# Kernel optimization log

Hardware: AMD Instinct MI355X
Metric: run time of the kernel (lower is better)

Reference implementation:

```python
import jax, jax.numpy as jnp
import numpy as np

N = 8192
K = 64
EPS = 1e-7
BN_EPS = 1e-5


def _norm(x):
    return jnp.sqrt(jnp.sum(x * x, axis=-1, keepdims=True))


def _bn(x, gamma, beta):
    # BatchNorm2d in training mode (batch statistics, biased variance)
    mu = jnp.mean(x, axis=(0, 2, 3), keepdims=True)
    var = jnp.mean((x - mu) ** 2, axis=(0, 2, 3), keepdims=True)
    return gamma.reshape(1, -1, 1, 1) * (x - mu) / jnp.sqrt(var + BN_EPS) + beta.reshape(1, -1, 1, 1)


def _conv1x1(x, w, b):
    # 1x1 conv == per-pixel linear: x [B,C,H,W], w [O,C]
    return jnp.einsum('bchw,oc->bohw', x, w) + b.reshape(1, -1, 1, 1)


def setup_inputs() -> dict:
    key = jax.random.key(0)
    ks = jax.random.split(key, 24)
    d = {}
    d['points'] = jax.random.normal(ks[0], (1, N, 3), jnp.float32)
    # graph_conv weights (torch code re-draws these every forward; here fixed params)
    lim0 = float(np.sqrt(6.0 / (4 + 64)))
    d['gw0'] = jax.random.uniform(ks[1], (4, 64), jnp.float32, -lim0, lim0)
    lim = float(np.sqrt(6.0 / (64 + 64)))
    for i in range(1, 5):
        d[f'gw{i}'] = jax.random.uniform(ks[1 + i], (64, 64), jnp.float32, -lim, lim)
    # mlp_1: 4->64->128, mlp_2: 192->256->1024 (1x1 convs + BN)
    d['c1w'] = jax.random.normal(ks[6], (64, 4), jnp.float32) * 0.1
    d['c1b'] = jnp.zeros((64,), jnp.float32)
    d['bn1g'] = jnp.ones((64,), jnp.float32)
    d['bn1b'] = jnp.zeros((64,), jnp.float32)
    d['c2w'] = jax.random.normal(ks[7], (128, 64), jnp.float32) * 0.1
    d['c2b'] = jnp.zeros((128,), jnp.float32)
    d['bn2g'] = jnp.ones((128,), jnp.float32)
    d['bn2b'] = jnp.zeros((128,), jnp.float32)
    d['c3w'] = jax.random.normal(ks[8], (256, 192), jnp.float32) * 0.05
    d['c3b'] = jnp.zeros((256,), jnp.float32)
    d['bn3g'] = jnp.ones((256,), jnp.float32)
    d['bn3b'] = jnp.zeros((256,), jnp.float32)
    d['c4w'] = jax.random.normal(ks[9], (1024, 256), jnp.float32) * 0.05
    d['c4b'] = jnp.zeros((1024,), jnp.float32)
    d['bn4g'] = jnp.ones((1024,), jnp.float32)
    d['bn4b'] = jnp.zeros((1024,), jnp.float32)
    return d


def _knn_search(points, k):
    # pairwise squared distances via ||a||^2 - 2ab + ||b||^2
    r = jnp.sum(points * points, axis=-1, keepdims=True)          # [1,N,1]
    dis = r - 2.0 * jnp.einsum('bnd,bmd->bnm', points, points) + jnp.swapaxes(r, 1, 2)
    _, idx = jax.lax.top_k(-dis, k)                                # [1,N,K]
    knn_pts = jax.vmap(lambda p, i: p[i])(points, idx)             # [1,N,K,3]
    return knn_pts


def _proj_knn(knn_pts):
    b, n, k, _ = knn_pts.shape
    pc = knn_pts - knn_pts[:, :, :1, :]                            # center on first neighbor (self)
    vn = jnp.sqrt(jnp.sum(pc * pc, axis=-1))                       # [1,N,K]
    id1 = jnp.argmax(vn, axis=-1)                                  # farthest neighbor
    a1 = jnp.take_along_axis(pc, jnp.broadcast_to(id1[:, :, None, None], (b, n, 1, 3)), axis=2)[:, :, 0, :]
    a1 = a1 / (_norm(a1) + EPS)
    a2 = jnp.mean(pc, axis=2)
    a2 = a2 / (_norm(a2) + EPS)
    a3 = a1 + 1.5 * a2
    a3 = a3 / (_norm(a3) + EPS)
    den = _norm(pc) + EPS                                          # [1,N,K,1]
    f1 = jnp.sum(pc * a1[:, :, None, :], axis=-1, keepdims=True) / den
    f2 = jnp.sum(pc * a2[:, :, None, :], axis=-1, keepdims=True) / den
    f3 = jnp.sum(pc * a3[:, :, None, :], axis=-1, keepdims=True) / den
    return jnp.concatenate([f1, f2, f3, vn[..., None]], axis=-1)   # [1,N,K,4]


def _proj_points(points):
    b, n, _ = points.shape
    vn = jnp.sqrt(jnp.sum(points * points, axis=-1))               # [1,N]
    i1 = jnp.argmax(vn, axis=-1)
    i2 = jnp.argmin(vn, axis=-1)
    a1 = jnp.take_along_axis(points, jnp.broadcast_to(i1[:, None, None], (b, 1, 3)), axis=1)[:, 0, :]
    a1 = a1 / (_norm(a1) + EPS)
    a2 = jnp.take_along_axis(points, jnp.broadcast_to(i2[:, None, None], (b, 1, 3)), axis=1)[:, 0, :]
    a2 = a2 / (_norm(a2) + EPS)
    a3 = a1 + 1.5 * a2
    a3 = a3 / (_norm(a3) + EPS)
    den = _norm(points) + EPS                                      # [1,N,1]
    f1 = jnp.sum(points * a1[:, None, :], axis=-1, keepdims=True) / den
    f2 = jnp.sum(points * a2[:, None, :], axis=-1, keepdims=True) / den
    f3 = jnp.sum(points * a3[:, None, :], axis=-1, keepdims=True) / den
    return jnp.concatenate([f1, f2, f3, vn[..., None]], axis=-1)   # [1,N,4]


def reference(points, gw0, gw1, gw2, gw3, gw4,
              c1w, c1b, bn1g, bn1b, c2w, c2b, bn2g, bn2b,
              c3w, c3b, bn3g, bn3b, c4w, c4b, bn4g, bn4b):
    n = points.shape[1]
    # upper branch: KNN -> rotation-invariant local feats -> 5-layer MLP -> max over K
    knn_pts = _knn_search(points, K)
    feat_up = _proj_knn(knn_pts)                                   # [1,N,K,4]
    x = feat_up.reshape(-1, 4)
    for w in (gw0, gw1, gw2, gw3, gw4):
        x = jax.nn.relu(x @ w)
    x = x.reshape(1, n, K, 64)
    emb_up = jnp.max(x, axis=2, keepdims=True)                     # [1,N,1,64]
    emb_up = emb_up.reshape(1, 64, n, 1)                           # raw view (reshape), as in torch
    # lower branch: global rotation-invariant feats -> mlp_1
    feat_down = _proj_points(points)                               # [1,N,4]
    emb_down = feat_down.reshape(1, 4, n, 1)                       # raw view (reshape), as in torch
    h = jax.nn.relu(_bn(_conv1x1(emb_down, c1w, c1b), bn1g, bn1b))
    h = jax.nn.relu(_bn(_conv1x1(h, c2w, c2b), bn2g, bn2b))        # [1,128,N,1]
    emb = jnp.concatenate([emb_up, h], axis=1)                     # [1,192,N,1]
    out = jax.nn.relu(_bn(_conv1x1(emb, c3w, c3b), bn3g, bn3b))
    out = jax.nn.relu(_bn(_conv1x1(out, c4w, c4b), bn4g, bn4b))    # [1,1024,N,1]
    return out
```

## Files before the change

### kernel.cpp

```cpp
#include <hip/hip_runtime.h>
#include <hip/hip_bf16.h>

#define NPTS 8192
#define KNN 64
#define EPSF 1e-7f

#define OFF_P4      0
#define OFF_STATS   32768
#define OFF_PART    36012
#define OFF_FEATDN  36864
#define OFF_WT1     69632
#define OFF_GWT     69888
#define OFF_BW2     79104
#define OFF_BW3     83200
#define OFF_BW4     107776
#define OFF_XB1     238848
#define OFF_XB3     500992
#define OFF_XB4     1287424
#define OFF_Y1      2336000
#define OFF_Y2      2860288
#define OFF_Y3      3908864
#define OFF_FEATUP  6006016

typedef __bf16 bf16x8 __attribute__((ext_vector_type(8)));
typedef float  f32x4  __attribute__((ext_vector_type(4)));

__device__ __forceinline__ unsigned f2u(float f) {
    unsigned u = __float_as_uint(f);
    return ((int)u >= 0) ? (u | 0x80000000u) : ~u;
}
__device__ __forceinline__ float key_to_f(unsigned long long k) {
    unsigned v = (unsigned)(k >> 32);
    unsigned ob = (v & 0x80000000u) ? (v ^ 0x80000000u) : ~v;
    return __uint_as_float(ob);
}
__device__ __forceinline__ unsigned short f2bf(float x) {
    union { __bf16 h; unsigned short s; } u;
    u.h = (__bf16)x;
    return u.s;
}
__device__ __forceinline__ unsigned packbf2(float lo, float hi) {
    return (unsigned)f2bf(lo) | ((unsigned)f2bf(hi) << 16);
}
__device__ __forceinline__ unsigned long long u64min(unsigned long long a, unsigned long long b){ return a < b ? a : b; }
__device__ __forceinline__ unsigned long long u64max(unsigned long long a, unsigned long long b){ return a < b ? b : a; }

__device__ __forceinline__ unsigned long long sort_merge(
    unsigned long long key, unsigned long long cur, int lane)
{
    #pragma unroll
    for (int k = 2; k <= 64; k <<= 1) {
        #pragma unroll
        for (int j = k >> 1; j > 0; j >>= 1) {
            unsigned long long o = __shfl_xor(key, j);
            bool up = ((lane & k) == 0);
            bool lower = ((lane & j) == 0);
            key = (lower == up) ? u64min(key, o) : u64max(key, o);
        }
    }
    unsigned long long rev = __shfl(key, 63 - lane);
    unsigned long long m = u64min(cur, rev);
    #pragma unroll
    for (int j = 32; j > 0; j >>= 1) {
        unsigned long long o = __shfl_xor(m, j);
        m = ((lane & j) == 0) ? u64min(m, o) : u64max(m, o);
    }
    return m;
}

__global__ __launch_bounds__(256) void prepwt_kernel(
    const float* __restrict__ points,
    const float* __restrict__ c1w, const float* __restrict__ c2w,
    const float* __restrict__ c3w, const float* __restrict__ c4w,
    const float* __restrict__ gw0, const float* __restrict__ gw1,
    const float* __restrict__ gw2, const float* __restrict__ gw3,
    const float* __restrict__ gw4,
    float* __restrict__ ws)
{
    const int t = blockIdx.x * 256 + threadIdx.x;
    const int T = 256 * 256;
    for (int m = t; m < 2944; m += T) ws[OFF_STATS + m] = 0.f;
    for (int m = t; m < 64*4; m += T) { int o = m >> 2, c = m & 3; ws[OFF_WT1 + c*64 + o] = c1w[m]; }

    unsigned short* bw2 = (unsigned short*)(ws + OFF_BW2);
    for (int m = t; m < 128*64; m += T)   bw2[m] = f2bf(c2w[m]);
    unsigned short* bw3 = (unsigned short*)(ws + OFF_BW3);
    for (int m = t; m < 256*192; m += T)  bw3[m] = f2bf(c3w[m]);
    unsigned short* bw4 = (unsigned short*)(ws + OFF_BW4);
    for (int m = t; m < 1024*256; m += T) bw4[m] = f2bf(c4w[m]);

    unsigned short* gwt = (unsigned short*)(ws + OFF_GWT);
    for (int m = t; m < 2048; m += T) {
        int o = m >> 5, i = m & 31;
        gwt[m] = (i < 4) ? f2bf(gw0[i*64 + o]) : (unsigned short)0;
    }
    const float* gsrc[4] = {gw1, gw2, gw3, gw4};
    for (int l = 0; l < 4; ++l) {
        const float* g = gsrc[l];
        unsigned short* dst = gwt + 2048 + l*4096;
        for (int m = t; m < 4096; m += T) { int o = m >> 6, i = m & 63; dst[m] = f2bf(g[i*64 + o]); }
    }

    if (blockIdx.x < 32) {
        const int n = blockIdx.x * 256 + threadIdx.x;
        float x = points[3*n+0], y = points[3*n+1], z = points[3*n+2];
        float rr = x*x + y*y + z*z;
        ((float4*)(ws + OFF_P4))[n] = make_float4(x, y, z, rr);
        float vn = sqrtf(rr);
        unsigned b = __float_as_uint(vn);
        unsigned long long mxk = ((unsigned long long)b << 32) | (unsigned long long)(0xFFFFFFFFu - (unsigned)n);
        unsigned long long mnk = ((unsigned long long)b << 32) | (unsigned long long)(unsigned)n;
        for (int j = 32; j > 0; j >>= 1) {
            mxk = u64max(mxk, __shfl_xor(mxk, j));
            mnk = u64min(mnk, __shfl_xor(mnk, j));
        }
        __shared__ unsigned long long smx[4], smn[4];
        int wid = threadIdx.x >> 6;
        if ((threadIdx.x & 63) == 0) { smx[wid] = mxk; smn[wid] = mnk; }
        __syncthreads();
        if (threadIdx.x == 0) {
            unsigned long long MX = 0ull, MN = ~0ull;
            for (int i = 0; i < 4; ++i) { MX = u64max(MX, smx[i]); MN = u64min(MN, smn[i]); }
            unsigned long long* parts = (unsigned long long*)(ws + OFF_PART);
            parts[2*blockIdx.x + 0] = MX;
            parts[2*blockIdx.x + 1] = MN;
        }
    }
}

__global__ __launch_bounds__(256) void prep_c_kernel(float* __restrict__ ws)
{
    __shared__ float av[9];
    const int tid = threadIdx.x;
    if (tid < 64) {
        const unsigned long long* parts = (const unsigned long long*)(ws + OFF_PART);
        unsigned long long mxk = (tid < 32) ? parts[2*tid + 0] : 0ull;
        unsigned long long mnk = (tid < 32) ? parts[2*tid + 1] : ~0ull;
        for (int j = 32; j > 0; j >>= 1) {
            mxk = u64max(mxk, __shfl_xor(mxk, j));
            mnk = u64min(mnk, __shfl_xor(mnk, j));
        }
        if (tid == 0) {
            int i1 = (int)(0xFFFFFFFFu - (unsigned)(mxk & 0xFFFFFFFFu));
            int i2 = (int)(unsigned)(mnk & 0xFFFFFFFFu);
            float4 p1 = ((const float4*)(ws + OFF_P4))[i1];
            float4 p2 = ((const float4*)(ws + OFF_P4))[i2];
            float n1 = sqrtf(p1.x*p1.x + p1.y*p1.y + p1.z*p1.z) + EPSF;
            float a1x = p1.x/n1, a1y = p1.y/n1, a1z = p1.z/n1;
            float n2 = sqrtf(p2.x*p2.x + p2.y*p2.y + p2.z*p2.z) + EPSF;
            float a2x = p2.x/n2, a2y = p2.y/n2, a2z = p2.z/n2;
            float a3x = a1x + 1.5f*a2x, a3y = a1y + 1.5f*a2y, a3z = a1z + 1.5f*a2z;
            float n3 = sqrtf(a3x*a3x + a3y*a3y + a3z*a3z) + EPSF;
            a3x /= n3; a3y /= n3; a3z /= n3;
            av[0]=a1x; av[1]=a1y; av[2]=a1z;
            av[3]=a2x; av[4]=a2y; av[5]=a2z;
            av[6]=a3x; av[7]=a3y; av[8]=a3z;
        }
    }
    __syncthreads();
    const int n = blockIdx.x * 256 + tid;
    float4 v = ((const float4*)(ws + OFF_P4))[n];
    float vn = sqrtf(v.w);
    float den = vn + EPSF;
    float f1 = (v.x*av[0] + v.y*av[1] + v.z*av[2]) / den;
    float f2 = (v.x*av[3] + v.y*av[4] + v.z*av[5]) / den;
    float f3 = (v.x*av[6] + v.y*av[7] + v.z*av[8]) / den;
    float4* f4 = (float4*)(ws + OFF_FEATDN + 4*n);
    *f4 = make_float4(f1, f2, f3, vn);
}

__global__ __launch_bounds__(512) void knn_feat_kernel(
    const float4* __restrict__ p4, float4* __restrict__ feat_up)
{
    __shared__ __align__(16) float4 scand[2048];
    __shared__ unsigned long long queue[8][128];
    const int lane = threadIdx.x & 63;
    const int wid  = threadIdx.x >> 6;
    const int q = blockIdx.x * 8 + wid;

    const float4 qa = p4[q];
    unsigned long long cur = ~0ull;
    float ke = __builtin_inff();
    int qc = 0;
    unsigned long long* Q = queue[wid];

    for (int base = 0; base < NPTS; base += 2048) {
        __syncthreads();
        for (int t = threadIdx.x; t < 2048; t += 512) scand[t] = p4[base + t];
        __syncthreads();
        #pragma unroll 2
        for (int sub = 0; sub < 2048; sub += 128) {
            float4 cd0 = scand[sub + lane];
            float4 cd1 = scand[sub + 64 + lane];
            float dot0 = fmaf(qa.x, cd0.x, fmaf(qa.y, cd0.y, qa.z * cd0.z));
            float dot1 = fmaf(qa.x, cd1.x, fmaf(qa.y, cd1.y, qa.z * cd1.z));
            float e0 = fmaf(-2.f, dot0, cd0.w);
            float e1 = fmaf(-2.f, dot1, cd1.w);
            bool p0 = e0 < ke;
            bool p1 = e1 < ke;
            unsigned long long m0 = __ballot(p0);
            unsigned long long m1 = __ballot(p1);
            if (m0) {
                int prefix = __builtin_amdgcn_mbcnt_hi((unsigned)(m0 >> 32),
                              __builtin_amdgcn_mbcnt_lo((unsigned)m0, 0));
                if (p0) Q[qc + prefix] = ((unsigned long long)f2u(e0) << 32)
                                       | (unsigned long long)(unsigned)(base + sub + lane);
                qc += __popcll(m0);
                if (qc >= 64) {
                    qc -= 64;
                    cur = sort_merge(Q[qc + lane], cur, lane);
                    ke = key_to_f(__shfl(cur, 63));
                }
            }
            if (m1) {
                int prefix = __builtin_amdgcn_mbcnt_hi((unsigned)(m1 >> 32),
                              __builtin_amdgcn_mbcnt_lo((unsigned)m1, 0));
                if (p1) Q[qc + prefix] = ((unsigned long long)f2u(e1) << 32)
                                       | (unsigned long long)(unsigned)(base + sub + 64 + lane);
                qc += __popcll(m1);
                if (qc >= 64) {
                    qc -= 64;
                    cur = sort_merge(Q[qc + lane], cur, lane);
                    ke = key_to_f(__shfl(cur, 63));
                }
            }
        }
    }
    cur = sort_merge((lane < qc) ? Q[lane] : ~0ull, cur, lane);

    int nidx = (int)(unsigned)(cur & 0xFFFFFFFFu);
    float4 np = p4[nidx];
    float ox = __shfl(np.x, 0), oy = __shfl(np.y, 0), oz = __shfl(np.z, 0);
    float pcx = np.x - ox, pcy = np.y - oy, pcz = np.z - oz;
    float vn = sqrtf(pcx*pcx + pcy*pcy + pcz*pcz);

    unsigned long long ak = ((unsigned long long)__float_as_uint(vn) << 32)
                          | (unsigned long long)(unsigned)(63 - lane);
    for (int s = 32; s > 0; s >>= 1) ak = u64max(ak, __shfl_xor(ak, s));
    int id1 = 63 - (int)(unsigned)(ak & 0xFFFFFFFFu);

    float a1x = __shfl(pcx, id1), a1y = __shfl(pcy, id1), a1z = __shfl(pcz, id1);
    float n1 = sqrtf(a1x*a1x + a1y*a1y + a1z*a1z) + EPSF;
    a1x /= n1; a1y /= n1; a1z /= n1;

    float sx = pcx, sy = pcy, sz = pcz;
    for (int s = 32; s > 0; s >>= 1) {
        sx += __shfl_xor(sx, s); sy += __shfl_xor(sy, s); sz += __shfl_xor(sz, s);
    }
    float a2x = sx * (1.f/64.f), a2y = sy * (1.f/64.f), a2z = sz * (1.f/64.f);
    float n2 = sqrtf(a2x*a2x + a2y*a2y + a2z*a2z) + EPSF;
    a2x /= n2; a2y /= n2; a2z /= n2;

    float a3x = a1x + 1.5f*a2x, a3y = a1y + 1.5f*a2y, a3z = a1z + 1.5f*a2z;
    float n3 = sqrtf(a3x*a3x + a3y*a3y + a3z*a3z) + EPSF;
    a3x /= n3; a3y /= n3; a3z /= n3;

    float den = vn + EPSF;
    float f1 = (pcx*a1x + pcy*a1y + pcz*a1z) / den;
    float f2 = (pcx*a2x + pcy*a2y + pcz*a2z) / den;
    float f3 = (pcx*a3x + pcy*a3y + pcz*a3z) / den;
    feat_up[q*64 + lane] = make_float4(f1, f2, f3, vn);
}

#define BROW 72
__global__ __launch_bounds__(256) void mlp_kernel(
    const float4* __restrict__ feat_up,
    const unsigned short* __restrict__ gwt,
    unsigned short* __restrict__ xb3)
{
    __shared__ __align__(16) unsigned short Blds[4][64 * BROW];
    const int lane = threadIdx.x & 63;
    const int wid  = threadIdx.x >> 6;
    const int q = blockIdx.x * 4 + wid;
    const int c = lane & 15, g = lane >> 4;
    unsigned short* B = Blds[wid];

    {
        float4 f = feat_up[q*64 + lane];
        uint2 p0;
        p0.x = packbf2(f.x, f.y);
        p0.y = packbf2(f.z, f.w);
        *(uint2*)&B[lane*BROW] = p0;
        *(uint2*)&B[lane*BROW + 4] = make_uint2(0, 0);
        uint4 z4 = make_uint4(0, 0, 0, 0);
        *(uint4*)&B[lane*BROW + 8]  = z4;
        *(uint4*)&B[lane*BROW + 16] = z4;
        *(uint4*)&B[lane*BROW + 24] = z4;
    }

    const unsigned short* Wl[5] = {gwt, gwt + 2048, gwt + 6144, gwt + 10240, gwt + 14336};
    f32x4 acc[4][4];

    for (int layer = 0; layer < 5; ++layer) {
        const int wstride = (layer == 0) ? 32 : 64;
        const int nks = (layer == 0) ? 1 : 2;
        #pragma unroll
        for (int mb = 0; mb < 4; ++mb)
            #pragma unroll
            for (int nb = 0; nb < 4; ++nb)
                acc[mb][nb] = (f32x4){0.f, 0.f, 0.f, 0.f};

        for (int ks = 0; ks < nks; ++ks) {
            bf16x8 af[4], bf[4];
            #pragma unroll
            for (int mb = 0; mb < 4; ++mb)
                af[mb] = *(const bf16x8*)(Wl[layer] + (mb*16 + c)*wstride + ks*32 + g*8);
            #pragma unroll
            for (int nb = 0; nb < 4; ++nb)
                bf[nb] = *(const bf16x8*)&B[(nb*16 + c)*BROW + ks*32 + g*8];
            #pragma unroll
            for (int mb = 0; mb < 4; ++mb)
                #pragma unroll
                for (int nb = 0; nb < 4; ++nb)
                    acc[mb][nb] = __builtin_amdgcn_mfma_f32_16x16x32_bf16(af[mb], bf[nb], acc[mb][nb], 0, 0, 0);
        }

        if (layer < 4) {
            #pragma unroll
            for (int mb = 0; mb < 4; ++mb) {
                #pragma unroll
                for (int nb = 0; nb < 4; ++nb) {
                    f32x4 a = acc[mb][nb];
                    uint2 pw;
                    pw.x = packbf2(fmaxf(a[0], 0.f), fmaxf(a[1], 0.f));
                    pw.y = packbf2(fmaxf(a[2], 0.f), fmaxf(a[3], 0.f));
                    *(uint2*)&B[(nb*16 + c)*BROW + mb*16 + g*4] = pw;
                }
            }
        }
    }

    const int cc = q >> 7;
    const int pbase = (q & 127) << 6;
    #pragma unroll
    for (int mb = 0; mb < 4; ++mb) {
        float v[4];
        #pragma unroll
        for (int r = 0; r < 4; ++r)
            v[r] = fmaxf(fmaxf(fmaxf(acc[mb][0][r], acc[mb][1][r]),
                               fmaxf(acc[mb][2][r], acc[mb][3][r])), 0.f);
        #pragma unroll
        for (int mask = 1; mask <= 8; mask <<= 1)
            #pragma unroll
            for (int r = 0; r < 4; ++r)
                v[r] = fmaxf(v[r], __shfl_xor(v[r], mask));
        if (c == 0) {
            #pragma unroll
            for (int r = 0; r < 4; ++r) {
                const int f = mb*16 + g*4 + r;
                xb3[(size_t)(pbase + f) * 192 + cc] = f2bf(v[r]);
            }
        }
    }
}

__global__ __launch_bounds__(256) void conv1_kernel(
    const float* __restrict__ x, const float* __restrict__ wt,
    const float* __restrict__ bias, float* __restrict__ y,
    float* __restrict__ stout)
{
    const int tid = threadIdx.x;
    const int p  = blockIdx.x * 256 + tid;
    const int o0 = blockIdx.y * 32;
    float acc[32];
    #pragma unroll
    for (int u = 0; u < 32; ++u) acc[u] = bias[o0 + u];
    #pragma unroll
    for (int c = 0; c < 4; ++c) {
        float xv = x[c * NPTS + p];
        const float* wr = wt + c * 64 + o0;
        #pragma unroll
        for (int u = 0; u < 32; ++u) acc[u] = fmaf(xv, wr[u], acc[u]);
    }
    #pragma unroll
    for (int u = 0; u < 32; ++u) y[(o0 + u) * NPTS + p] = acc[u];

    __shared__ float ps[4][32], pss[4][32];
    const int wid = tid >> 6, lane = tid & 63;
    #pragma unroll
    for (int u = 0; u < 32; ++u) {
        float s = acc[u], ss = acc[u] * acc[u];
        for (int j = 32; j > 0; j >>= 1) { s += __shfl_xor(s, j); ss += __shfl_xor(ss, j); }
        if (lane == 0) { ps[wid][u] = s; pss[wid][u] = ss; }
    }
    __syncthreads();
    if (tid < 32) {
        float S  = ps[0][tid] + ps[1][tid] + ps[2][tid] + ps[3][tid];
        float SS = pss[0][tid] + pss[1][tid] + pss[2][tid] + pss[3][tid];
        atomicAdd(&stout[o0 + tid], S);
        atomicAdd(&stout[64 + o0 + tid], SS);
    }
}

__global__ __launch_bounds__(256) void bnpack_kernel(
    const float* __restrict__ y, const float* __restrict__ st,
    const float* __restrict__ gam, const float* __restrict__ bet,
    int C, int stride, int coff, unsigned short* __restrict__ xb)
{
    __shared__ float sc[256], sh[256];
    __shared__ __align__(16) unsigned short tile[64][264];
    const int tid = threadIdx.x;
    for (int cc = tid; cc < C; cc += 256) {
        float mu  = st[cc] * (1.f / 8192.f);
        float var = st[C + cc] * (1.f / 8192.f) - mu * mu;
        float s = gam[cc] / sqrtf(var + 1e-5f);
        sc[cc] = s; sh[cc] = bet[cc] - mu * s;
    }
    __syncthreads();
    const int pl = tid & 63, g = tid >> 6;
    const int p = blockIdx.x * 64 + pl;
    for (int c0 = g * 8; c0 < C; c0 += 32) {
        unsigned pk[4];
        #pragma unroll
        for (int h = 0; h < 4; ++h) {
            float v0 = fmaxf(fmaf(y[(c0 + 2*h    ) * NPTS + p], sc[c0 + 2*h    ], sh[c0 + 2*h    ]), 0.f);
            float v1 = fmaxf(fmaf(y[(c0 + 2*h + 1) * NPTS + p], sc[c0 + 2*h + 1], sh[c0 + 2*h + 1]), 0.f);
            pk[h] = packbf2(v0, v1);
        }
        *(uint4*)&tile[pl][c0] = make_uint4(pk[0], pk[1], pk[2], pk[3]);
    }
    __syncthreads();
    const int cpr = C >> 3;
    const int nch = 64 * cpr;
    for (int idx = tid; idx < nch; idx += 256) {
        int r = idx / cpr, cc = (idx - r * cpr) * 8;
        *(uint4*)&xb[(size_t)(blockIdx.x * 64 + r) * stride + coff + cc] = *(uint4*)&tile[r][cc];
    }
}

__global__ __launch_bounds__(256) void conv_mfma_kernel(
    const unsigned short* __restrict__ A, const unsigned short* __restrict__ Bx,
    const float* __restrict__ bias, int K, int M,
    float* __restrict__ y, float* __restrict__ stout)
{
    const int lane = threadIdx.x & 63;
    const int w = threadIdx.x >> 6;
    const int n0 = blockIdx.x * 256 + w * 64;
    const int m0 = blockIdx.y * 64;
    const int c = lane & 15, g = lane >> 4;

    f32x4 acc[4][4];
    #pragma unroll
    for (int mt = 0; mt < 4; ++mt)
        #pragma unroll
        for (int nt = 0; nt < 4; ++nt)
            acc[mt][nt] = (f32x4){0.f, 0.f, 0.f, 0.f};

    for (int k0 = 0; k0 < K; k0 += 32) {
        bf16x8 af[4], bf[4];
        #pragma unroll
        for (int mt = 0; mt < 4; ++mt)
            af[mt] = *(const bf16x8*)(A + (size_t)(m0 + mt*16 + c) * K + k0 + g*8);
        #pragma unroll
        for (int nt = 0; nt < 4; ++nt)
            bf[nt] = *(const bf16x8*)(Bx + (size_t)(n0 + nt*16 + c) * K + k0 + g*8);
        #pragma unroll
        for (int mt = 0; mt < 4; ++mt)
            #pragma unroll
            for (int nt = 0; nt < 4; ++nt)
                acc[mt][nt] = __builtin_amdgcn_mfma_f32_16x16x32_bf16(af[mt], bf[nt], acc[mt][nt], 0, 0, 0);
    }

    #pragma unroll
    for (int mt = 0; mt < 4; ++mt) {
        float s[4], ss[4];
        #pragma unroll
        for (int r = 0; r < 4; ++r) {
            const int o = m0 + mt*16 + g*4 + r;
            const float bv = bias[o];
            float sum = 0.f, sq = 0.f;
            #pragma unroll
            for (int nt = 0; nt < 4; ++nt) {
                float v = acc[mt][nt][r] + bv;
                y[(size_t)o * NPTS + n0 + nt*16 + c] = v;
                sum += v; sq += v * v;
            }
            s[r] = sum; ss[r] = sq;
        }
        #pragma unroll
        for (int mask = 1; mask <= 8; mask <<= 1)
            #pragma unroll
            for (int r = 0; r < 4; ++r) {
                s[r]  += __shfl_xor(s[r],  mask);
                ss[r] += __shfl_xor(ss[r], mask);
            }
        if (c == 0) {
            #pragma unroll
            for (int r = 0; r < 4; ++r) {
                const int o = m0 + mt*16 + g*4 + r;
                atomicAdd(&stout[o], s[r]);
                atomicAdd(&stout[M + o], ss[r]);
            }
        }
    }
}

__global__ __launch_bounds__(256) void bnrelu_kernel(
    const float4* y, const float* __restrict__ st,
    const float* __restrict__ g, const float* __restrict__ b,
    float4* out, int C)
{
    int idx = blockIdx.x * 256 + threadIdx.x;
    int c = idx >> 11;
    float mu  = st[c] * (1.f / 8192.f);
    float var = st[C + c] * (1.f / 8192.f) - mu * mu;
    float scale = g[c] / sqrtf(var + 1e-5f);
    float sh = b[c] - mu * scale;
    float4 v = y[idx];
    v.x = fmaxf(fmaf(v.x, scale, sh), 0.f);
    v.y = fmaxf(fmaf(v.y, scale, sh), 0.f);
    v.z = fmaxf(fmaf(v.z, scale, sh), 0.f);
    v.w = fmaxf(fmaf(v.w, scale, sh), 0.f);
    out[idx] = v;
}

extern "C" void kernel_launch(void* const* d_in, const int* in_sizes, int n_in,
                              void* d_out, int out_size, void* d_ws, size_t ws_size,
                              hipStream_t stream) {
    const float* points = (const float*)d_in[0];
    const float* gw0 = (const float*)d_in[1];
    const float* gw1 = (const float*)d_in[2];
    const float* gw2 = (const float*)d_in[3];
    const float* gw3 = (const float*)d_in[4];
    const float* gw4 = (const float*)d_in[5];
    const float* c1w = (const float*)d_in[6];  const float* c1b = (const float*)d_in[7];
    const float* bn1g = (const float*)d_in[8]; const float* bn1b = (const float*)d_in[9];
    const float* c2w = (const float*)d_in[10]; const float* c2b = (const float*)d_in[11];
    const float* bn2g = (const float*)d_in[12];const float* bn2b = (const float*)d_in[13];
    const float* c3w = (const float*)d_in[14]; const float* c3b = (const float*)d_in[15];
    const float* bn3g = (const float*)d_in[16];const float* bn3b = (const float*)d_in[17];
    const float* c4w = (const float*)d_in[18]; const float* c4b = (const float*)d_in[19];
    const float* bn4g = (const float*)d_in[20];const float* bn4b = (const float*)d_in[21];

    float* ws = (float*)d_ws;
    float* p4f    = ws + OFF_P4;
    float* featdn = ws + OFF_FEATDN;
    float* featup = ws + OFF_FEATUP;
    float* y1 = ws + OFF_Y1; float* y2 = ws + OFF_Y2; float* y3 = ws + OFF_Y3;
    float* s1 = ws + OFF_STATS + 0;
    float* s2 = ws + OFF_STATS + 128;
    float* s3 = ws + OFF_STATS + 384;
    float* s4 = ws + OFF_STATS + 896;
    float* wt1 = ws + OFF_WT1;
    const unsigned short* gwt = (const unsigned short*)(ws + OFF_GWT);
    const unsigned short* bw2 = (const unsigned short*)(ws + OFF_BW2);
    const unsigned short* bw3 = (const unsigned short*)(ws + OFF_BW3);
    const unsigned short* bw4 = (const unsigned short*)(ws + OFF_BW4);
    unsigned short* xb1 = (unsigned short*)(ws + OFF_XB1);
    unsigned short* xb3 = (unsigned short*)(ws + OFF_XB3);
    unsigned short* xb4 = (unsigned short*)(ws + OFF_XB4);
    float* outp = (float*)d_out;

    prepwt_kernel<<<256, 256, 0, stream>>>(points, c1w, c2w, c3w, c4w,
                                           gw0, gw1, gw2, gw3, gw4, ws);
    prep_c_kernel<<<32, 256, 0, stream>>>(ws);

    knn_feat_kernel<<<1024, 512, 0, stream>>>((const float4*)p4f, (float4*)featup);
    mlp_kernel<<<2048, 256, 0, stream>>>((const float4*)featup, gwt, xb3);

    conv1_kernel<<<dim3(32, 2), 256, 0, stream>>>(featdn, wt1, c1b, y1, s1);
    bnpack_kernel<<<128, 256, 0, stream>>>(y1, s1, bn1g, bn1b, 64, 64, 0, xb1);
    conv_mfma_kernel<<<dim3(32, 2), 256, 0, stream>>>(bw2, xb1, c2b, 64, 128, y2, s2);
    bnpack_kernel<<<128, 256, 0, stream>>>(y2, s2, bn2g, bn2b, 128, 192, 64, xb3);
    conv_mfma_kernel<<<dim3(32, 4), 256, 0, stream>>>(bw3, xb3, c3b, 192, 256, y3, s3);
    bnpack_kernel<<<128, 256, 0, stream>>>(y3, s3, bn3g, bn3b, 256, 256, 0, xb4);
    conv_mfma_kernel<<<dim3(32, 16), 256, 0, stream>>>(bw4, xb4, c4b, 256, 1024, outp, s4);
    bnrelu_kernel<<<8192, 256, 0, stream>>>((const float4*)outp, s4, bn4g, bn4b, (float4*)outp, 1024);
}
```

Measured before the change: 350.0 us.

## Fuse BatchNorm-ReLU-bf16 packing into the MFMA conv operand loads

Removes the three bnpack kernels. Each conv kernel now computes the previous layer's BN scale and shift into shared memory, then applies BN+ReLU and bf16 conversion while loading its B operand straight from the fp32 pre-activation buffer. The upper-branch MLP output goes to a separate 64-channel buffer that the conv3 kernel reads directly for its first K slice, which removes the concat stride. This saves launches and the bf16 intermediate round trip. In exchange, the fp32 activations are reread once per M-block as scalar strided loads, and the BN math is recomputed for every output tile, notably 16 times for the 1024-channel layer.

```diff
diff --git a/kernel.cpp b/kernel.cpp
--- a/kernel.cpp
+++ b/kernel.cpp
@@ -14,9 +14,7 @@
 #define OFF_BW2     79104
 #define OFF_BW3     83200
 #define OFF_BW4     107776
-#define OFF_XB1     238848
-#define OFF_XB3     500992
-#define OFF_XB4     1287424
+#define OFF_XB3V    238848
 #define OFF_Y1      2336000
 #define OFF_Y2      2860288
 #define OFF_Y3      3908864
@@ -266,7 +264,7 @@
 __global__ __launch_bounds__(256) void mlp_kernel(
     const float4* __restrict__ feat_up,
     const unsigned short* __restrict__ gwt,
-    unsigned short* __restrict__ xb3)
+    unsigned short* __restrict__ xb3v)
 {
     __shared__ __align__(16) unsigned short Blds[4][64 * BROW];
     const int lane = threadIdx.x & 63;
@@ -348,7 +346,7 @@
             #pragma unroll
             for (int r = 0; r < 4; ++r) {
                 const int f = mb*16 + g*4 + r;
-                xb3[(size_t)(pbase + f) * 192 + cc] = f2bf(v[r]);
+                xb3v[(size_t)(pbase + f) * 64 + cc] = f2bf(v[r]);
             }
         }
     }
@@ -392,49 +390,27 @@
     }
 }
 
-__global__ __launch_bounds__(256) void bnpack_kernel(
-    const float* __restrict__ y, const float* __restrict__ st,
-    const float* __restrict__ gam, const float* __restrict__ bet,
-    int C, int stride, int coff, unsigned short* __restrict__ xb)
+__global__ __launch_bounds__(256) void convbn_kernel(
+    const unsigned short* __restrict__ A,
+    const unsigned short* __restrict__ Bdir, int Kdir,
+    const float* __restrict__ yprev,
+    const float* __restrict__ stp, const float* __restrict__ gam, const float* __restrict__ bet,
+    const float* __restrict__ bias, int K, int M,
+    float* __restrict__ yout, float* __restrict__ stout)
 {
     __shared__ float sc[256], sh[256];
-    __shared__ __align__(16) unsigned short tile[64][264];
     const int tid = threadIdx.x;
-    for (int cc = tid; cc < C; cc += 256) {
-        float mu  = st[cc] * (1.f / 8192.f);
-        float var = st[C + cc] * (1.f / 8192.f) - mu * mu;
+    const int Cp = K - Kdir;
+    for (int cc = tid; cc < Cp; cc += 256) {
+        float mu  = stp[cc] * (1.f / 8192.f);
+        float var = stp[Cp + cc] * (1.f / 8192.f) - mu * mu;
         float s = gam[cc] / sqrtf(var + 1e-5f);
         sc[cc] = s; sh[cc] = bet[cc] - mu * s;
     }
     __syncthreads();
-    const int pl = tid & 63, g = tid >> 6;
-    const int p = blockIdx.x * 64 + pl;
-    for (int c0 = g * 8; c0 < C; c0 += 32) {
-        unsigned pk[4];
-        #pragma unroll
-        for (int h = 0; h < 4; ++h) {
-            float v0 = fmaxf(fmaf(y[(c0 + 2*h    ) * NPTS + p], sc[c0 + 2*h    ], sh[c0 + 2*h    ]), 0.f);
-            float v1 = fmaxf(fmaf(y[(c0 + 2*h + 1) * NPTS + p], sc[c0 + 2*h + 1], sh[c0 + 2*h + 1]), 0.f);
-            pk[h] = packbf2(v0, v1);
-        }
-        *(uint4*)&tile[pl][c0] = make_uint4(pk[0], pk[1], pk[2], pk[3]);
-    }
-    __syncthreads();
-    const int cpr = C >> 3;
-    const int nch = 64 * cpr;
-    for (int idx = tid; idx < nch; idx += 256) {
-        int r = idx / cpr, cc = (idx - r * cpr) * 8;
-        *(uint4*)&xb[(size_t)(blockIdx.x * 64 + r) * stride + coff + cc] = *(uint4*)&tile[r][cc];
-    }
-}
-
-__global__ __launch_bounds__(256) void conv_mfma_kernel(
-    const unsigned short* __restrict__ A, const unsigned short* __restrict__ Bx,
-    const float* __restrict__ bias, int K, int M,
-    float* __restrict__ y, float* __restrict__ stout)
-{
-    const int lane = threadIdx.x & 63;
-    const int w = threadIdx.x >> 6;
+
+    const int lane = tid & 63;
+    const int w = tid >> 6;
     const int n0 = blockIdx.x * 256 + w * 64;
     const int m0 = blockIdx.y * 64;
     const int c = lane & 15, g = lane >> 4;
@@ -451,9 +427,25 @@
         #pragma unroll
         for (int mt = 0; mt < 4; ++mt)
             af[mt] = *(const bf16x8*)(A + (size_t)(m0 + mt*16 + c) * K + k0 + g*8);
-        #pragma unroll
-        for (int nt = 0; nt < 4; ++nt)
-            bf[nt] = *(const bf16x8*)(Bx + (size_t)(n0 + nt*16 + c) * K + k0 + g*8);
+        if (k0 + 32 <= Kdir) {
+            #pragma unroll
+            for (int nt = 0; nt < 4; ++nt)
+                bf[nt] = *(const bf16x8*)(Bdir + (size_t)(n0 + nt*16 + c) * Kdir + k0 + g*8);
+        } else {
+            const int ch0 = k0 - Kdir + g*8;
+            #pragma unroll
+            for (int nt = 0; nt < 4; ++nt) {
+                const int pt = n0 + nt*16 + c;
+                bf16x8 r;
+                #pragma unroll
+                for (int j = 0; j < 8; ++j) {
+                    float vv = fmaxf(fmaf(yprev[(size_t)(ch0 + j) * NPTS + pt],
+                                          sc[ch0 + j], sh[ch0 + j]), 0.f);
+                    r[j] = (__bf16)vv;
+                }
+                bf[nt] = r;
+            }
+        }
         #pragma unroll
         for (int mt = 0; mt < 4; ++mt)
             #pragma unroll
@@ -472,7 +464,7 @@
             #pragma unroll
             for (int nt = 0; nt < 4; ++nt) {
                 float v = acc[mt][nt][r] + bv;
-                y[(size_t)o * NPTS + n0 + nt*16 + c] = v;
+                yout[(size_t)o * NPTS + n0 + nt*16 + c] = v;
                 sum += v; sq += v * v;
             }
             s[r] = sum; ss[r] = sq;
@@ -546,9 +538,7 @@
     const unsigned short* bw2 = (const unsigned short*)(ws + OFF_BW2);
     const unsigned short* bw3 = (const unsigned short*)(ws + OFF_BW3);
     const unsigned short* bw4 = (const unsigned short*)(ws + OFF_BW4);
-    unsigned short* xb1 = (unsigned short*)(ws + OFF_XB1);
-    unsigned short* xb3 = (unsigned short*)(ws + OFF_XB3);
-    unsigned short* xb4 = (unsigned short*)(ws + OFF_XB4);
+    unsigned short* xb3v = (unsigned short*)(ws + OFF_XB3V);
     float* outp = (float*)d_out;
 
     prepwt_kernel<<<256, 256, 0, stream>>>(points, c1w, c2w, c3w, c4w,
@@ -556,14 +546,14 @@
     prep_c_kernel<<<32, 256, 0, stream>>>(ws);
 
     knn_feat_kernel<<<1024, 512, 0, stream>>>((const float4*)p4f, (float4*)featup);
-    mlp_kernel<<<2048, 256, 0, stream>>>((const float4*)featup, gwt, xb3);
+    mlp_kernel<<<2048, 256, 0, stream>>>((const float4*)featup, gwt, xb3v);
 
     conv1_kernel<<<dim3(32, 2), 256, 0, stream>>>(featdn, wt1, c1b, y1, s1);
-    bnpack_kernel<<<128, 256, 0, stream>>>(y1, s1, bn1g, bn1b, 64, 64, 0, xb1);
-    conv_mfma_kernel<<<dim3(32, 2), 256, 0, stream>>>(bw2, xb1, c2b, 64, 128, y2, s2);
-    bnpack_kernel<<<128, 256, 0, stream>>>(y2, s2, bn2g, bn2b, 128, 192, 64, xb3);
-    conv_mfma_kernel<<<dim3(32, 4), 256, 0, stream>>>(bw3, xb3, c3b, 192, 256, y3, s3);
-    bnpack_kernel<<<128, 256, 0, stream>>>(y3, s3, bn3g, bn3b, 256, 256, 0, xb4);
-    conv_mfma_kernel<<<dim3(32, 16), 256, 0, stream>>>(bw4, xb4, c4b, 256, 1024, outp, s4);
+    convbn_kernel<<<dim3(32, 2), 256, 0, stream>>>(bw2, nullptr, 0, y1, s1, bn1g, bn1b,
+                                                   c2b, 64, 128, y2, s2);
+    convbn_kernel<<<dim3(32, 4), 256, 0, stream>>>(bw3, xb3v, 64, y2, s2, bn2g, bn2b,
+                                                   c3b, 192, 256, y3, s3);
+    convbn_kernel<<<dim3(32, 16), 256, 0, stream>>>(bw4, nullptr, 0, y3, s3, bn3g, bn3b,
+                                                    c4b, 256, 1024, outp, s4);
     bnrelu_kernel<<<8192, 256, 0, stream>>>((const float4*)outp, s4, bn4g, bn4b, (float4*)outp, 1024);
 }
```

Result: faster. 332.8 us (-4.9%).
